# Kernel optimization log

Measured on AMD Instinct MI355X. Metric: run time of the kernel, lower is better.

Reference implementation:

```python
import jax, jax.numpy as jnp
import numpy as np

N = 50000          # nodes
E = 800000         # edges
F = 128            # input features
H = 4              # heads
C = 16             # out_channels per head (h_dim // 2)
HC = H * C         # 64, concatenated hidden size
G = 128            # graphs in batch
NCLS = 10


def _lin(key, fan_in, fan_out):
    kw, kb = jax.random.split(key)
    scale = 1.0 / np.sqrt(fan_in)
    W = jax.random.uniform(kw, (fan_in, fan_out), minval=-scale, maxval=scale, dtype=jnp.float32)
    b = jax.random.uniform(kb, (fan_out,), minval=-scale, maxval=scale, dtype=jnp.float32)
    return W, b


def setup_inputs() -> dict:
    key = jax.random.key(0)
    ks = jax.random.split(key, 20)
    inp = {
        'x': jax.random.normal(ks[0], (N, F), dtype=jnp.float32),
        'edge_index': jax.random.randint(ks[1], (2, E), 0, N, dtype=jnp.int32),
        'batch_mapping': jnp.sort(jax.random.randint(ks[2], (N,), 0, G, dtype=jnp.int32)),
    }
    fan_ins = [F, HC, HC]
    ki = 3
    for layer, fin in enumerate(fan_ins, start=1):
        for nm in ('Wq', 'Wk', 'Wv', 'Ws'):
            Wmat, bvec = _lin(ks[ki], fin, HC); ki += 1
            inp[f'{nm}{layer}'] = Wmat
            inp[f'b{nm[1]}{layer}'] = bvec
    Wl, bl = _lin(ks[ki], HC, NCLS)
    inp['W_lin'] = Wl
    inp['b_lin'] = bl
    return inp


def _transformer_conv(x, src, dst, Wq, bq, Wk, bk, Wv, bv, Ws, bs):
    n = x.shape[0]
    q = (x @ Wq + bq).reshape(n, H, C)   # [N,H,C]
    k = (x @ Wk + bk).reshape(n, H, C)
    v = (x @ Wv + bv).reshape(n, H, C)
    # per-edge attention scores, softmax-normalized per destination node
    score = jnp.einsum('ehc,ehc->eh', q[dst], k[src]) / jnp.sqrt(jnp.asarray(C, x.dtype))  # [E,H]
    m = jax.ops.segment_max(score, dst, num_segments=n)          # [N,H]
    p = jnp.exp(score - m[dst])                                   # [E,H]
    denom = jax.ops.segment_sum(p, dst, num_segments=n)           # [N,H]
    alpha = p / (denom[dst] + 1e-16)
    agg = jax.ops.segment_sum(alpha[:, :, None] * v[src], dst, num_segments=n)  # [N,H,C]
    return agg.reshape(n, HC) + x @ Ws + bs  # root/skip connection


def reference(x, edge_index, batch_mapping,
              Wq1, bq1, Wk1, bk1, Wv1, bv1, Ws1, bs1,
              Wq2, bq2, Wk2, bk2, Wv2, bv2, Ws2, bs2,
              Wq3, bq3, Wk3, bk3, Wv3, bv3, Ws3, bs3,
              W_lin, b_lin):
    src, dst = edge_index[0], edge_index[1]
    h = jax.nn.relu(_transformer_conv(x, src, dst, Wq1, bq1, Wk1, bk1, Wv1, bv1, Ws1, bs1))
    h = jax.nn.relu(_transformer_conv(h, src, dst, Wq2, bq2, Wk2, bk2, Wv2, bv2, Ws2, bs2))
    h = _transformer_conv(h, src, dst, Wq3, bq3, Wk3, bk3, Wv3, bv3, Ws3, bs3)
    # global mean pool per graph
    counts = jax.ops.segment_sum(jnp.ones((h.shape[0],), h.dtype), batch_mapping, num_segments=G)
    pooled = jax.ops.segment_sum(h, batch_mapping, num_segments=G) / jnp.maximum(counts, 1.0)[:, None]
    logits = pooled @ W_lin + b_lin
    return jax.nn.softmax(logits, axis=1)
```

## Files before the change

kernel.cpp:

```cpp
#include <hip/hip_runtime.h>
#include <hip/hip_fp16.h>
#include <math.h>

#define N_NODES 50000
#define NPAD    50048
#define N_EDGES 800000
#define F_IN    128
#define HC      64
#define NG      128
#define NCLS    10
#define NXT     782
#define XCHUNK  98
#define DRANGE  6250
#define SCB     2048
#define MAXDEG  64

typedef __attribute__((ext_vector_type(8))) _Float16 f16x8;
typedef __attribute__((ext_vector_type(4))) float f32x4;
typedef _Float16 half2v __attribute__((ext_vector_type(2)));

__device__ __forceinline__ float fdot2_acc(unsigned a, unsigned b, float c) {
#if __has_builtin(__builtin_amdgcn_fdot2)
    half2v ha, hb;
    __builtin_memcpy(&ha, &a, 4);
    __builtin_memcpy(&hb, &b, 4);
    return __builtin_amdgcn_fdot2(ha, hb, c, false);
#else
    __half2 ha = *(__half2*)&a, hb = *(__half2*)&b;
    return c + __low2float(ha) * __low2float(hb) + __high2float(ha) * __high2float(hb);
#endif
}

__device__ __forceinline__ void ell_body(int bid, const int* __restrict__ src,
                                         const int* __restrict__ dst,
                                         int* __restrict__ deg,
                                         int* __restrict__ slots) {
    int grp = bid & 7;
    int nb = SCB >> 3;
    int slot = bid >> 3;
    int lo = grp * DRANGE, hi = lo + DRANGE;
    const int4* d4p = (const int4*)dst;
    const int4* s4p = (const int4*)src;
    int nchunks = N_EDGES >> 2;
    for (int t = slot * 256 + (int)threadIdx.x; t < nchunks; t += nb * 256) {
        int4 d = d4p[t];
        int4 s = s4p[t];
        if (d.x >= lo && d.x < hi) { int r = atomicAdd(&deg[d.x], 1); if (r < MAXDEG) slots[d.x * MAXDEG + r] = s.x; }
        if (d.y >= lo && d.y < hi) { int r = atomicAdd(&deg[d.y], 1); if (r < MAXDEG) slots[d.y * MAXDEG + r] = s.y; }
        if (d.z >= lo && d.z < hi) { int r = atomicAdd(&deg[d.z], 1); if (r < MAXDEG) slots[d.z * MAXDEG + r] = s.z; }
        if (d.w >= lo && d.w < hi) { int r = atomicAdd(&deg[d.w], 1); if (r < MAXDEG) slots[d.w * MAXDEG + r] = s.w; }
    }
}

__global__ __launch_bounds__(256) void ellconv_kernel(
    const int* __restrict__ src, const int* __restrict__ dst,
    int* __restrict__ deg, int* __restrict__ slots,
    const float* __restrict__ x, unsigned short* __restrict__ xf16, int n4x,
    const float* __restrict__ W10, const float* __restrict__ W11,
    const float* __restrict__ W12, const float* __restrict__ W13,
    const float* __restrict__ W20, const float* __restrict__ W21,
    const float* __restrict__ W22, const float* __restrict__ W23,
    const float* __restrict__ W30, const float* __restrict__ W31,
    const float* __restrict__ W32, const float* __restrict__ W33,
    unsigned short* __restrict__ wt_h)
{
    int bid = blockIdx.x;
    if (bid < SCB) {
        ell_body(bid, src, dst, deg, slots);
    } else if (bid < SCB + 256) {
        int idx = (bid - SCB) * 256 + threadIdx.x;
        const float* W;
        int K, dbase, rr;
        if (idx < 32768) {
            int mat = idx >> 13; rr = idx & 8191; K = 128;
            W = (mat == 0) ? W10 : (mat == 1) ? W11 : (mat == 2) ? W12 : W13;
            dbase = 0 * 32768 + mat * 8192;
        } else if (idx < 49152) {
            int i2 = idx - 32768;
            int mat = i2 >> 12; rr = i2 & 4095; K = 64;
            W = (mat == 0) ? W20 : (mat == 1) ? W21 : (mat == 2) ? W22 : W23;
            dbase = 1 * 32768 + mat * 4096;
        } else {
            int i3 = idx - 49152;
            int mat = i3 >> 12; rr = i3 & 4095; K = 64;
            W = (mat == 0) ? W30 : (mat == 1) ? W31 : (mat == 2) ? W32 : W33;
            dbase = 2 * 32768 + mat * 4096;
        }
        int k = rr >> 6, c = rr & 63;
        float f = W[k * 64 + c];
        wt_h[dbase + c * K + k] = __half_as_ushort(__float2half_rn(f));
    } else {
        int t = (bid - SCB - 256) * 256 + threadIdx.x;
        if (t < n4x) {
            float4 f = ((const float4*)x)[t];
            ushort4 u;
            u.x = __half_as_ushort(__float2half_rn(f.x));
            u.y = __half_as_ushort(__float2half_rn(f.y));
            u.z = __half_as_ushort(__float2half_rn(f.z));
            u.w = __half_as_ushort(__float2half_rn(f.w));
            ((ushort4*)xf16)[t] = u;
        }
    }
}

__device__ __forceinline__ void gemm_epilogue(int y, int row0, int w, int lr, int kq,
    f32x4* acc,
    const float* __restrict__ b0, const float* __restrict__ b1,
    const float* __restrict__ b2, const float* __restrict__ b3,
    unsigned short* __restrict__ qp16, float* __restrict__ sf,
    unsigned short* __restrict__ kvpk, int M)
{
    const float* bias = (y == 0) ? b0 : (y == 1) ? b1 : (y == 2) ? b2 : b3;
    if (y == 3) {
        #pragma unroll
        for (int f = 0; f < 4; ++f) {
            float bv = bias[f * 16 + lr];
            #pragma unroll
            for (int r = 0; r < 4; ++r) {
                int gr = row0 + w * 16 + kq * 4 + r;
                if (gr < M) sf[(size_t)gr * 64 + f * 16 + lr] = acc[f][r] + bv;
            }
        }
    } else if (y == 0) {
        #pragma unroll
        for (int f = 0; f < 4; ++f) {
            float bv = bias[f * 16 + lr];
            #pragma unroll
            for (int r = 0; r < 4; ++r) {
                int gr = row0 + w * 16 + kq * 4 + r;
                if (gr < M)
                    qp16[(size_t)gr * 64 + f * 16 + lr] =
                        __half_as_ushort(__float2half_rn(acc[f][r] + bv));
            }
        }
    } else {
        int off = (y == 1) ? 0 : 64;
        #pragma unroll
        for (int f = 0; f < 4; ++f) {
            float bv = bias[f * 16 + lr];
            #pragma unroll
            for (int r = 0; r < 4; ++r) {
                int gr = row0 + w * 16 + kq * 4 + r;
                if (gr < M)
                    kvpk[(size_t)gr * 128 + off + f * 16 + lr] =
                        __half_as_ushort(__float2half_rn(acc[f][r] + bv));
            }
        }
    }
}

__global__ __launch_bounds__(256) void mfma_gemm_kernel(
    const unsigned short* __restrict__ A16, const unsigned short* __restrict__ Wt_h,
    const float* __restrict__ b0, const float* __restrict__ b1,
    const float* __restrict__ b2, const float* __restrict__ b3,
    unsigned short* __restrict__ qp16, float* __restrict__ sf,
    unsigned short* __restrict__ kvpk, int M, int K)
{
    extern __shared__ char smem[];
    int bid = blockIdx.x;
    int xcd = bid & 7;
    int slot = bid >> 3;
    int xt = xcd * XCHUNK + (slot >> 2);
    int y = slot & 3;
    if (xt >= NXT) return;
    int row0 = xt * 64;

    const int tileB = 64 * K * 2;
    char* sA  = smem;
    char* sBh = smem + tileB;

    int tid = threadIdx.x;
    int cpr = K >> 3;
    int total = 64 * cpr;
    const f16x8* gA  = (const f16x8*)(A16 + (size_t)row0 * K);
    const f16x8* gBh = (const f16x8*)(Wt_h + (size_t)y * 64 * K);
    for (int t = tid; t < total; t += 256) {
        int row = t / cpr, cs = t - row * cpr;
        int dstB = row * (K * 2) + ((cs * 16) ^ ((row & 7) << 4));
        *(f16x8*)(sA + dstB)  = gA[t];
        *(f16x8*)(sBh + dstB) = gBh[t];
    }
    __syncthreads();

    int w = tid >> 6, lane = tid & 63, lr = lane & 15, kq = lane >> 4;
    f32x4 acc[4];
    #pragma unroll
    for (int f = 0; f < 4; ++f) acc[f] = (f32x4){0.f, 0.f, 0.f, 0.f};

    int arow = w * 16 + lr;
    int abase = arow * (K * 2);
    int aswz = (arow & 7) << 4;
    for (int ks = 0; ks < K; ks += 32) {
        int kb = ks * 2 + kq * 16;
        f16x8 a = *(const f16x8*)(sA + abase + (kb ^ aswz));
        #pragma unroll
        for (int f = 0; f < 4; ++f) {
            int brow = f * 16 + lr;
            int boff = brow * (K * 2) + (kb ^ ((brow & 7) << 4));
            f16x8 bh = *(const f16x8*)(sBh + boff);
            acc[f] = __builtin_amdgcn_mfma_f32_16x16x32_f16(a, bh, acc[f], 0, 0, 0);
        }
    }
    gemm_epilogue(y, row0, w, lr, kq, acc, b0, b1, b2, b3, qp16, sf, kvpk, M);
}

__global__ __launch_bounds__(256) void attn_kernel(
    const unsigned short* __restrict__ qp, const float* __restrict__ sf,
    const uint4* __restrict__ kv4,
    const int* __restrict__ deg, const int* __restrict__ slots,
    float* __restrict__ hout,
    unsigned short* __restrict__ h16,
    int n, int mode)
{
    __shared__ float lds[4][64 * 17];
    int node = (int)((blockIdx.x * (size_t)blockDim.x + threadIdx.x) >> 6);
    int lane = threadIdx.x & 63;
    int wl = threadIdx.x >> 6;
    if (node >= n) return;
    int h = lane >> 4, j = lane & 15;

    const uint4* q4 = (const uint4*)(qp + (size_t)node * 64 + h * 16);
    uint4 qa = q4[0], qb = q4[1];

    int dg = deg[node];
    if (dg > MAXDEG) dg = MAXDEG;
    const int* row = slots + (size_t)node * MAXDEG;
    float acc[16];
    #pragma unroll
    for (int c = 0; c < 16; ++c) acc[c] = 0.f;
    float dsum = 0.f;

    for (int eb = 0; eb < dg; eb += 16) {
        int e = eb + j;
        int ec = (e < dg) ? e : (dg - 1);
        int src = row[ec];
        const uint4* kvr = kv4 + (size_t)src * 16 + h * 2;
        uint4 ka = kvr[0], kb = kvr[1];
        uint4 va = kvr[8], vb = kvr[9];
        float s = 0.f;
        s = fdot2_acc(qa.x, ka.x, s);
        s = fdot2_acc(qa.y, ka.y, s);
        s = fdot2_acc(qa.z, ka.z, s);
        s = fdot2_acc(qa.w, ka.w, s);
        s = fdot2_acc(qb.x, kb.x, s);
        s = fdot2_acc(qb.y, kb.y, s);
        s = fdot2_acc(qb.z, kb.z, s);
        s = fdot2_acc(qb.w, kb.w, s);
        float p = (e < dg) ? __expf(s * 0.25f) : 0.f;
        dsum += p;
        unsigned uv[8] = {va.x, va.y, va.z, va.w, vb.x, vb.y, vb.z, vb.w};
        #pragma unroll
        for (int i = 0; i < 8; ++i) {
            __half2 hv = *(__half2*)&uv[i];
            acc[2 * i]     += p * __low2float(hv);
            acc[2 * i + 1] += p * __high2float(hv);
        }
    }

    dsum += __shfl_xor(dsum, 1, 64);
    dsum += __shfl_xor(dsum, 2, 64);
    dsum += __shfl_xor(dsum, 4, 64);
    dsum += __shfl_xor(dsum, 8, 64);
    float inv = 1.f / (dsum + 1e-16f);

    float* L = lds[wl];
    int wb = lane * 17;
    #pragma unroll
    for (int c = 0; c < 16; ++c) L[wb + c] = acc[c];
    __builtin_amdgcn_wave_barrier();
    float sum = 0.f;
    int rb = (h * 16) * 17 + j;
    #pragma unroll
    for (int jj = 0; jj < 16; ++jj) sum += L[rb + jj * 17];

    float outv = sum * inv + sf[(size_t)node * 64 + lane];
    if (mode == 1) {
        outv = fmaxf(outv, 0.f);
        h16[(size_t)node * 64 + lane] = __half_as_ushort(__float2half_rn(outv));
    } else {
        hout[(size_t)node * 64 + lane] = outv;
    }
}

__global__ __launch_bounds__(256) void poolhead_kernel(
    const float* __restrict__ h, const int* __restrict__ bm,
    const float* __restrict__ Wl, const float* __restrict__ bl,
    float* __restrict__ out)
{
    int g = blockIdx.x;
    int lo = 0, hi = N_NODES;
    while (lo < hi) { int mid = (lo + hi) >> 1; if (bm[mid] < g) lo = mid + 1; else hi = mid; }
    int s = lo;
    lo = 0; hi = N_NODES;
    while (lo < hi) { int mid = (lo + hi) >> 1; if (bm[mid] < g + 1) lo = mid + 1; else hi = mid; }
    int e = lo;

    int c = threadIdx.x & 63, sub = threadIdx.x >> 6;
    float sum = 0.f;
    for (int i = s + sub; i < e; i += 4) sum += h[(size_t)i * 64 + c];
    __shared__ float tmp[256];
    __shared__ float pl[64];
    tmp[threadIdx.x] = sum;
    __syncthreads();
    if (sub == 0) {
        sum = tmp[c] + tmp[c + 64] + tmp[c + 128] + tmp[c + 192];
        int cnt = e - s;
        pl[c] = sum / fmaxf((float)cnt, 1.0f);
    }
    __syncthreads();
    if (threadIdx.x < 64) {
        int lane = threadIdx.x;
        float logit = -INFINITY;
        if (lane < NCLS) {
            float acc = bl[lane];
            for (int k = 0; k < 64; ++k) acc += pl[k] * Wl[k * NCLS + lane];
            logit = acc;
        }
        float mx = logit;
        mx = fmaxf(mx, __shfl_xor(mx, 1, 64));
        mx = fmaxf(mx, __shfl_xor(mx, 2, 64));
        mx = fmaxf(mx, __shfl_xor(mx, 4, 64));
        mx = fmaxf(mx, __shfl_xor(mx, 8, 64));
        float ex = (lane < NCLS) ? __expf(logit - mx) : 0.f;
        float sm = ex;
        sm += __shfl_xor(sm, 1, 64);
        sm += __shfl_xor(sm, 2, 64);
        sm += __shfl_xor(sm, 4, 64);
        sm += __shfl_xor(sm, 8, 64);
        if (lane < NCLS) out[g * NCLS + lane] = ex / sm;
    }
}

extern "C" void kernel_launch(void* const* d_in, const int* in_sizes, int n_in,
                              void* d_out, int out_size, void* d_ws, size_t ws_size,
                              hipStream_t stream) {
    const float* x  = (const float*)d_in[0];
    const int*   ei = (const int*)d_in[1];
    const int*   bm = (const int*)d_in[2];
    const float* W1[4] = {(const float*)d_in[3], (const float*)d_in[5], (const float*)d_in[7], (const float*)d_in[9]};
    const float* B1[4] = {(const float*)d_in[4], (const float*)d_in[6], (const float*)d_in[8], (const float*)d_in[10]};
    const float* W2[4] = {(const float*)d_in[11], (const float*)d_in[13], (const float*)d_in[15], (const float*)d_in[17]};
    const float* B2[4] = {(const float*)d_in[12], (const float*)d_in[14], (const float*)d_in[16], (const float*)d_in[18]};
    const float* W3[4] = {(const float*)d_in[19], (const float*)d_in[21], (const float*)d_in[23], (const float*)d_in[25]};
    const float* B3[4] = {(const float*)d_in[20], (const float*)d_in[22], (const float*)d_in[24], (const float*)d_in[26]};
    const float* Wl = (const float*)d_in[27];
    const float* bl = (const float*)d_in[28];
    float* outp = (float*)d_out;

    float* sf     = (float*)d_ws;
    float* hf     = sf + (size_t)NPAD * 64;
    unsigned short* qp16 = (unsigned short*)(hf + (size_t)NPAD * 64);
    unsigned short* kvpk = qp16 + (size_t)NPAD * 64;
    unsigned short* xf16 = kvpk + (size_t)NPAD * 128;
    unsigned short* hs16 = xf16 + (size_t)NPAD * 128;
    unsigned short* wt_h = hs16 + (size_t)NPAD * 64;
    int* deg     = (int*)(wt_h + 3 * 32768);
    int* slots   = deg + N_NODES;

    const int* srcp = ei;
    const int* dstp = ei + N_EDGES;

    int n4x = N_NODES * F_IN / 4;
    int ggrid = 8 * XCHUNK * 4;
    int agrid = (N_NODES + 3) / 4;
    size_t smem1  = (size_t)2 * 64 * F_IN * 2;
    size_t smem23 = (size_t)2 * 64 * HC * 2;

    hipMemsetAsync(deg, 0, N_NODES * sizeof(int), stream);

    int ecgrid = SCB + 256 + (n4x + 255) / 256;
    ellconv_kernel<<<ecgrid, 256, 0, stream>>>(
        srcp, dstp, deg, slots,
        x, xf16, n4x,
        W1[0], W1[1], W1[2], W1[3],
        W2[0], W2[1], W2[2], W2[3],
        W3[0], W3[1], W3[2], W3[3],
        wt_h);

    mfma_gemm_kernel<<<ggrid, 256, smem1, stream>>>(xf16,
        wt_h + 0 * 32768,
        B1[0], B1[1], B1[2], B1[3], qp16, sf, kvpk, N_NODES, F_IN);
    attn_kernel<<<agrid, 256, 0, stream>>>(qp16, sf, (const uint4*)kvpk, deg, slots,
                                           nullptr, hs16, N_NODES, 1);
    mfma_gemm_kernel<<<ggrid, 256, smem23, stream>>>(hs16,
        wt_h + 1 * 32768,
        B2[0], B2[1], B2[2], B2[3], qp16, sf, kvpk, N_NODES, HC);
    attn_kernel<<<agrid, 256, 0, stream>>>(qp16, sf, (const uint4*)kvpk, deg, slots,
                                           nullptr, hs16, N_NODES, 1);
    mfma_gemm_kernel<<<ggrid, 256, smem23, stream>>>(hs16,
        wt_h + 2 * 32768,
        B3[0], B3[1], B3[2], B3[3], qp16, sf, kvpk, N_NODES, HC);
    attn_kernel<<<agrid, 256, 0, stream>>>(qp16, sf, (const uint4*)kvpk, deg, slots,
                                           hf, nullptr, N_NODES, 0);

    poolhead_kernel<<<NG, 256, 0, stream>>>(hf, bm, Wl, bl, outp);
}
```

Measured before the change: 240.1 us.

## Store skip projection in fp16, skip src loads for out-of-range edges, guard attention loads

The skip-connection projection is now written and read as fp16 instead of fp32, which halves its store and load traffic in each GEMM and attention pass. The ELL build kernel skips loading the src chunk when none of the four destinations fall in the block's range, cutting redundant src reads across the 8 range groups. The attention loop now skips padded edge lanes entirely instead of clamping them to the last edge and reloading its K/V. The costs are extra fp16 rounding on the skip term and more divergent branching.

```diff
diff --git a/kernel.cpp b/kernel.cpp
--- a/kernel.cpp
+++ b/kernel.cpp
@@ -44,11 +44,16 @@
     int nchunks = N_EDGES >> 2;
     for (int t = slot * 256 + (int)threadIdx.x; t < nchunks; t += nb * 256) {
         int4 d = d4p[t];
+        bool v0 = (d.x >= lo && d.x < hi);
+        bool v1 = (d.y >= lo && d.y < hi);
+        bool v2 = (d.z >= lo && d.z < hi);
+        bool v3 = (d.w >= lo && d.w < hi);
+        if (!(v0 | v1 | v2 | v3)) continue;
         int4 s = s4p[t];
-        if (d.x >= lo && d.x < hi) { int r = atomicAdd(&deg[d.x], 1); if (r < MAXDEG) slots[d.x * MAXDEG + r] = s.x; }
-        if (d.y >= lo && d.y < hi) { int r = atomicAdd(&deg[d.y], 1); if (r < MAXDEG) slots[d.y * MAXDEG + r] = s.y; }
-        if (d.z >= lo && d.z < hi) { int r = atomicAdd(&deg[d.z], 1); if (r < MAXDEG) slots[d.z * MAXDEG + r] = s.z; }
-        if (d.w >= lo && d.w < hi) { int r = atomicAdd(&deg[d.w], 1); if (r < MAXDEG) slots[d.w * MAXDEG + r] = s.w; }
+        if (v0) { int r = atomicAdd(&deg[d.x], 1); if (r < MAXDEG) slots[d.x * MAXDEG + r] = s.x; }
+        if (v1) { int r = atomicAdd(&deg[d.y], 1); if (r < MAXDEG) slots[d.y * MAXDEG + r] = s.y; }
+        if (v2) { int r = atomicAdd(&deg[d.z], 1); if (r < MAXDEG) slots[d.z * MAXDEG + r] = s.z; }
+        if (v3) { int r = atomicAdd(&deg[d.w], 1); if (r < MAXDEG) slots[d.w * MAXDEG + r] = s.w; }
     }
 }
 
@@ -107,21 +112,12 @@
     f32x4* acc,
     const float* __restrict__ b0, const float* __restrict__ b1,
     const float* __restrict__ b2, const float* __restrict__ b3,
-    unsigned short* __restrict__ qp16, float* __restrict__ sf,
+    unsigned short* __restrict__ qp16, unsigned short* __restrict__ sf16,
     unsigned short* __restrict__ kvpk, int M)
 {
     const float* bias = (y == 0) ? b0 : (y == 1) ? b1 : (y == 2) ? b2 : b3;
-    if (y == 3) {
-        #pragma unroll
-        for (int f = 0; f < 4; ++f) {
-            float bv = bias[f * 16 + lr];
-            #pragma unroll
-            for (int r = 0; r < 4; ++r) {
-                int gr = row0 + w * 16 + kq * 4 + r;
-                if (gr < M) sf[(size_t)gr * 64 + f * 16 + lr] = acc[f][r] + bv;
-            }
-        }
-    } else if (y == 0) {
+    if (y == 0 || y == 3) {
+        unsigned short* dstp = (y == 0) ? qp16 : sf16;
         #pragma unroll
         for (int f = 0; f < 4; ++f) {
             float bv = bias[f * 16 + lr];
@@ -129,7 +125,7 @@
             for (int r = 0; r < 4; ++r) {
                 int gr = row0 + w * 16 + kq * 4 + r;
                 if (gr < M)
-                    qp16[(size_t)gr * 64 + f * 16 + lr] =
+                    dstp[(size_t)gr * 64 + f * 16 + lr] =
                         __half_as_ushort(__float2half_rn(acc[f][r] + bv));
             }
         }
@@ -153,7 +149,7 @@
     const unsigned short* __restrict__ A16, const unsigned short* __restrict__ Wt_h,
     const float* __restrict__ b0, const float* __restrict__ b1,
     const float* __restrict__ b2, const float* __restrict__ b3,
-    unsigned short* __restrict__ qp16, float* __restrict__ sf,
+    unsigned short* __restrict__ qp16, unsigned short* __restrict__ sf16,
     unsigned short* __restrict__ kvpk, int M, int K)
 {
     extern __shared__ char smem[];
@@ -201,11 +197,11 @@
             acc[f] = __builtin_amdgcn_mfma_f32_16x16x32_f16(a, bh, acc[f], 0, 0, 0);
         }
     }
-    gemm_epilogue(y, row0, w, lr, kq, acc, b0, b1, b2, b3, qp16, sf, kvpk, M);
+    gemm_epilogue(y, row0, w, lr, kq, acc, b0, b1, b2, b3, qp16, sf16, kvpk, M);
 }
 
 __global__ __launch_bounds__(256) void attn_kernel(
-    const unsigned short* __restrict__ qp, const float* __restrict__ sf,
+    const unsigned short* __restrict__ qp, const unsigned short* __restrict__ sf16,
     const uint4* __restrict__ kv4,
     const int* __restrict__ deg, const int* __restrict__ slots,
     float* __restrict__ hout,
@@ -232,28 +228,29 @@
 
     for (int eb = 0; eb < dg; eb += 16) {
         int e = eb + j;
-        int ec = (e < dg) ? e : (dg - 1);
-        int src = row[ec];
-        const uint4* kvr = kv4 + (size_t)src * 16 + h * 2;
-        uint4 ka = kvr[0], kb = kvr[1];
-        uint4 va = kvr[8], vb = kvr[9];
-        float s = 0.f;
-        s = fdot2_acc(qa.x, ka.x, s);
-        s = fdot2_acc(qa.y, ka.y, s);
-        s = fdot2_acc(qa.z, ka.z, s);
-        s = fdot2_acc(qa.w, ka.w, s);
-        s = fdot2_acc(qb.x, kb.x, s);
-        s = fdot2_acc(qb.y, kb.y, s);
-        s = fdot2_acc(qb.z, kb.z, s);
-        s = fdot2_acc(qb.w, kb.w, s);
-        float p = (e < dg) ? __expf(s * 0.25f) : 0.f;
-        dsum += p;
-        unsigned uv[8] = {va.x, va.y, va.z, va.w, vb.x, vb.y, vb.z, vb.w};
-        #pragma unroll
-        for (int i = 0; i < 8; ++i) {
-            __half2 hv = *(__half2*)&uv[i];
-            acc[2 * i]     += p * __low2float(hv);
-            acc[2 * i + 1] += p * __high2float(hv);
+        if (e < dg) {
+            int src = row[e];
+            const uint4* kvr = kv4 + (size_t)src * 16 + h * 2;
+            uint4 ka = kvr[0], kb = kvr[1];
+            uint4 va = kvr[8], vb = kvr[9];
+            float s = 0.f;
+            s = fdot2_acc(qa.x, ka.x, s);
+            s = fdot2_acc(qa.y, ka.y, s);
+            s = fdot2_acc(qa.z, ka.z, s);
+            s = fdot2_acc(qa.w, ka.w, s);
+            s = fdot2_acc(qb.x, kb.x, s);
+            s = fdot2_acc(qb.y, kb.y, s);
+            s = fdot2_acc(qb.z, kb.z, s);
+            s = fdot2_acc(qb.w, kb.w, s);
+            float p = __expf(s * 0.25f);
+            dsum += p;
+            unsigned uv[8] = {va.x, va.y, va.z, va.w, vb.x, vb.y, vb.z, vb.w};
+            #pragma unroll
+            for (int i = 0; i < 8; ++i) {
+                __half2 hv = *(__half2*)&uv[i];
+                acc[2 * i]     += p * __low2float(hv);
+                acc[2 * i + 1] += p * __high2float(hv);
+            }
         }
     }
 
@@ -273,7 +270,8 @@
     #pragma unroll
     for (int jj = 0; jj < 16; ++jj) sum += L[rb + jj * 17];
 
-    float outv = sum * inv + sf[(size_t)node * 64 + lane];
+    float skip = __half2float(__ushort_as_half(sf16[(size_t)node * 64 + lane]));
+    float outv = sum * inv + skip;
     if (mode == 1) {
         outv = fmaxf(outv, 0.f);
         h16[(size_t)node * 64 + lane] = __half_as_ushort(__float2half_rn(outv));
@@ -347,10 +345,10 @@
     const float* bl = (const float*)d_in[28];
     float* outp = (float*)d_out;
 
-    float* sf     = (float*)d_ws;
-    float* hf     = sf + (size_t)NPAD * 64;
+    float* hf     = (float*)d_ws;
     unsigned short* qp16 = (unsigned short*)(hf + (size_t)NPAD * 64);
-    unsigned short* kvpk = qp16 + (size_t)NPAD * 64;
+    unsigned short* sf16 = qp16 + (size_t)NPAD * 64;
+    unsigned short* kvpk = sf16 + (size_t)NPAD * 64;
     unsigned short* xf16 = kvpk + (size_t)NPAD * 128;
     unsigned short* hs16 = xf16 + (size_t)NPAD * 128;
     unsigned short* wt_h = hs16 + (size_t)NPAD * 64;
@@ -379,18 +377,18 @@
 
     mfma_gemm_kernel<<<ggrid, 256, smem1, stream>>>(xf16,
         wt_h + 0 * 32768,
-        B1[0], B1[1], B1[2], B1[3], qp16, sf, kvpk, N_NODES, F_IN);
-    attn_kernel<<<agrid, 256, 0, stream>>>(qp16, sf, (const uint4*)kvpk, deg, slots,
+        B1[0], B1[1], B1[2], B1[3], qp16, sf16, kvpk, N_NODES, F_IN);
+    attn_kernel<<<agrid, 256, 0, stream>>>(qp16, sf16, (const uint4*)kvpk, deg, slots,
                                            nullptr, hs16, N_NODES, 1);
     mfma_gemm_kernel<<<ggrid, 256, smem23, stream>>>(hs16,
         wt_h + 1 * 32768,
-        B2[0], B2[1], B2[2], B2[3], qp16, sf, kvpk, N_NODES, HC);
-    attn_kernel<<<agrid, 256, 0, stream>>>(qp16, sf, (const uint4*)kvpk, deg, slots,
+        B2[0], B2[1], B2[2], B2[3], qp16, sf16, kvpk, N_NODES, HC);
+    attn_kernel<<<agrid, 256, 0, stream>>>(qp16, sf16, (const uint4*)kvpk, deg, slots,
                                            nullptr, hs16, N_NODES, 1);
     mfma_gemm_kernel<<<ggrid, 256, smem23, stream>>>(hs16,
         wt_h + 2 * 32768,
-        B3[0], B3[1], B3[2], B3[3], qp16, sf, kvpk, N_NODES, HC);
-    attn_kernel<<<agrid, 256, 0, stream>>>(qp16, sf, (const uint4*)kvpk, deg, slots,
+        B3[0], B3[1], B3[2], B3[3], qp16, sf16, kvpk, N_NODES, HC);
+    attn_kernel<<<agrid, 256, 0, stream>>>(qp16, sf16, (const uint4*)kvpk, deg, slots,
                                            hf, nullptr, N_NODES, 0);
 
     poolhead_kernel<<<NG, 256, 0, stream>>>(hf, bm, Wl, bl, outp);
```

Measured after the change: 240.5 us (median of 2 runs). About the same (+0.1%).
